# Optimization experiments

Hardware: AMD Instinct MI355X
Metric: run time of the kernel (lower is better)

Reference implementation:

```python
import jax, jax.numpy as jnp
import numpy as np

H = 8          # num_heads
EPS = 1e-6     # layernorm epsilon
NEG_INF = -1e9


def _ln(x, g, b):
    m = jnp.mean(x, axis=-1, keepdims=True)
    v = jnp.mean(jnp.square(x - m), axis=-1, keepdims=True)
    return g * (x - m) * jax.lax.rsqrt(v + EPS) + b


def _mha(xq, kv, wq, wk, wv, wo, bias):
    # xq: [B,Tq,D], kv: [B,Tk,D]; weights [D,D]. Returns (out [B,Tq,D], weights [B,H,Tq,Tk]).
    B, Tq, D = xq.shape
    dh = D // H
    q = (xq @ wq) * (dh ** -0.5)
    k = kv @ wk
    v = kv @ wv
    q = q.reshape(B, Tq, H, dh).transpose(0, 2, 1, 3)
    k = k.reshape(B, -1, H, dh).transpose(0, 2, 1, 3)
    v = v.reshape(B, -1, H, dh).transpose(0, 2, 1, 3)
    logits = jnp.einsum('bhqd,bhkd->bhqk', q, k)
    if bias is not None:
        logits = logits + bias
    w = jax.nn.softmax(logits, axis=-1)
    out = jnp.einsum('bhqk,bhkd->bhqd', w, v).transpose(0, 2, 1, 3).reshape(B, Tq, D)
    return out @ wo, w


def setup_inputs() -> dict:
    key = jax.random.key(0)
    ks = jax.random.split(key, 16)
    B, Td, Te, D, F, L = 2, 2048, 2048, 512, 2048, 2
    s = 0.02
    inp = {
        'x': jax.random.normal(ks[0], (B, Td, D), jnp.float32),
        'enc_a': jax.random.normal(ks[1], (B, Te, D), jnp.float32),
        'enc_c': jax.random.normal(ks[2], (B, Te, D), jnp.float32),
        'sa_wq': jax.random.normal(ks[3], (L, D, D), jnp.float32) * s,
        'sa_wk': jax.random.normal(ks[4], (L, D, D), jnp.float32) * s,
        'sa_wv': jax.random.normal(ks[5], (L, D, D), jnp.float32) * s,
        'sa_wo': jax.random.normal(ks[6], (L, D, D), jnp.float32) * s,
        'ed_wq': jax.random.normal(ks[7], (L, D, D), jnp.float32) * s,
        'ed_wk': jax.random.normal(ks[8], (L, D, D), jnp.float32) * s,
        'ed_wv': jax.random.normal(ks[9], (L, D, D), jnp.float32) * s,
        'ed_wo': jax.random.normal(ks[10], (L, D, D), jnp.float32) * s,
        'ffn_w1': jax.random.normal(ks[11], (L, D, F), jnp.float32) * s,
        'ffn_w2': jax.random.normal(ks[12], (L, F, D), jnp.float32) * s,
        'ln1_g': jnp.ones((L, D), jnp.float32), 'ln1_b': jnp.zeros((L, D), jnp.float32),
        'ln2_g': jnp.ones((L, D), jnp.float32), 'ln2_b': jnp.zeros((L, D), jnp.float32),
        'ln3_g': jnp.ones((L, D), jnp.float32), 'ln3_b': jnp.zeros((L, D), jnp.float32),
        'out_g': jnp.ones((D,), jnp.float32), 'out_b': jnp.zeros((D,), jnp.float32),
    }
    return inp


def reference(x, enc_a, enc_c, sa_wq, sa_wk, sa_wv, sa_wo, ed_wq, ed_wk, ed_wv, ed_wo,
              ffn_w1, ffn_w2, ln1_g, ln1_b, ln2_g, ln2_b, ln3_g, ln3_b, out_g, out_b):
    B, T, D = x.shape
    L = sa_wq.shape[0]
    # decoder self-attention causal bias, broadcast over [B,H]
    causal = jnp.where(jnp.tril(jnp.ones((T, T), bool)), 0.0, NEG_INF)[None, None]
    avg = None
    for i in range(L):
        h = _ln(x, ln1_g[i], ln1_b[i])
        y, _ = _mha(h, h, sa_wq[i], sa_wk[i], sa_wv[i], sa_wo[i], causal)
        x = x + y  # residual (dropout inactive at eval)
        h = _ln(x, ln2_g[i], ln2_b[i])
        y0, _ = _mha(h, enc_a, ed_wq[i], ed_wk[i], ed_wv[i], ed_wo[i], None)
        y1, w = _mha(h, enc_c, ed_wq[i], ed_wk[i], ed_wv[i], ed_wo[i], None)
        # original overwrites attn_scores with second call's head-averaged weights
        scores = jnp.mean(w, axis=1) / L
        avg = scores if avg is None else avg + scores
        x = x + y0 + y1
        h = _ln(x, ln3_g[i], ln3_b[i])
        x = x + jax.nn.relu(h @ ffn_w1[i]) @ ffn_w2[i]
    x = _ln(x, out_g, out_b)
    return x, avg
```

## Files before the change

### kernel.cpp

```cpp
#include <hip/hip_runtime.h>
#include <hip/hip_bf16.h>

#define BB 2
#define TT 2048
#define DD 512
#define FF 2048
#define HH 8
#define DH 64
#define LL 2
#define MM (BB*TT)

typedef __attribute__((ext_vector_type(8))) short bf16x8;
typedef __attribute__((ext_vector_type(4))) float f32x4;

__device__ __forceinline__ float bf2f(unsigned short u) {
    return __uint_as_float(((unsigned int)u) << 16);
}
__device__ __forceinline__ unsigned short f2bf(float f) {
    unsigned int u = __float_as_uint(f);
    u += 0x7fffu + ((u >> 16) & 1u);
    return (unsigned short)(u >> 16);
}
__device__ __forceinline__ unsigned int cvtpk(float a, float b) {
    unsigned int r;
    asm("v_cvt_pk_bf16_f32 %0, %1, %2" : "=v"(r) : "v"(a), "v"(b));
    return r;
}
__device__ __forceinline__ void gload16(const void* g, void* l) {
    __builtin_amdgcn_global_load_lds((__attribute__((address_space(1))) void*)g,
                                     (__attribute__((address_space(3))) void*)l, 16, 0, 0);
}

template<bool BF16OUT>
__global__ __launch_bounds__(256) void ln_kernel(const float* __restrict__ x,
                                                 const float* __restrict__ g,
                                                 const float* __restrict__ b,
                                                 void* __restrict__ out)
{
    const int row = blockIdx.x;
    const int tid = threadIdx.x;
    const float2 v = ((const float2*)(x + (size_t)row * DD))[tid];
    float s = v.x + v.y;
    float q = v.x * v.x + v.y * v.y;
    #pragma unroll
    for (int off = 32; off; off >>= 1) {
        s += __shfl_down(s, off);
        q += __shfl_down(q, off);
    }
    __shared__ float ss[4], qq[4];
    const int wid = tid >> 6;
    if ((tid & 63) == 0) { ss[wid] = s; qq[wid] = q; }
    __syncthreads();
    s = ss[0] + ss[1] + ss[2] + ss[3];
    q = qq[0] + qq[1] + qq[2] + qq[3];
    const float mean = s * (1.0f / DD);
    const float var = q * (1.0f / DD) - mean * mean;
    const float inv = rsqrtf(var + 1e-6f);
    const float2 gg = ((const float2*)g)[tid];
    const float2 bb = ((const float2*)b)[tid];
    const float ox = gg.x * (v.x - mean) * inv + bb.x;
    const float oy = gg.y * (v.y - mean) * inv + bb.y;
    if (BF16OUT) {
        const unsigned int pk = cvtpk(ox, oy);
        ((unsigned int*)((unsigned short*)out + (size_t)row * DD))[tid] = pk;
    } else {
        float2 o; o.x = ox; o.y = oy;
        ((float2*)((float*)out + (size_t)row * DD))[tid] = o;
    }
}

struct CvtEJob { const float* s; unsigned short* d; };
struct CvtEJobs2 { CvtEJob j[2]; };

__global__ __launch_bounds__(256) void cvt_kernel(CvtEJobs2 P, int n)
{
    const CvtEJob jb = P.j[blockIdx.z];
    const int i = (blockIdx.x * 256 + threadIdx.x) * 8;
    if (i >= n) return;
    const float4 a = *(const float4*)(jb.s + i);
    const float4 b = *(const float4*)(jb.s + i + 4);
    unsigned int o[4];
    o[0] = cvtpk(a.x, a.y); o[1] = cvtpk(a.z, a.w);
    o[2] = cvtpk(b.x, b.y); o[3] = cvtpk(b.z, b.w);
    *(bf16x8*)(jb.d + i) = *(bf16x8*)o;
}

struct CvtTJob { const float* s; unsigned short* d; int K; int N; };
struct CvtTJobs20 { CvtTJob j[20]; };

__global__ __launch_bounds__(256) void cvtT_kernel(CvtTJobs20 P)
{
    __shared__ float t[32][33];
    const CvtTJob jb = P.j[blockIdx.z];
    const int gk = blockIdx.y << 5, gn = blockIdx.x << 5;
    if (gk >= jb.K || gn >= jb.N) return;
    const int tx = threadIdx.x & 31, ty = threadIdx.x >> 5;
    #pragma unroll
    for (int i = 0; i < 4; ++i)
        t[ty + i * 8][tx] = jb.s[(size_t)(gk + ty + i * 8) * jb.N + gn + tx];
    __syncthreads();
    #pragma unroll
    for (int i = 0; i < 4; ++i)
        jb.d[(size_t)(gn + ty + i * 8) * jb.K + gk + tx] = f2bf(t[tx][ty + i * 8]);
}

struct GemmJob {
    const unsigned short* A;
    const unsigned short* Wt;
    const float* res;
    float* Cf;
    unsigned short* Cb;
    unsigned short* Ct;
    float scale;
    int relu;
};
struct GemmJobs6 { GemmJob j[6]; };

__global__ __launch_bounds__(256, 2) void gemm_mfma(GemmJobs6 P, int M, int N, int K)
{
    __shared__ __align__(16) unsigned char lds[32768];
    const GemmJob jb = P.j[blockIdx.z];
    const int tid = threadIdx.x, lane = tid & 63, w = tid >> 6;
    const int bn = blockIdx.x << 7, bm = blockIdx.y << 7;
    const int wr = (w >> 1) << 6, wc = (w & 1) << 6;
    const size_t strA = (size_t)K * 2;

    f32x4 acc[4][4] = {};
    const int akey = (lane & 7) << 4;
    const int frow = lane & 15;
    const int kq = (lane >> 4) << 4;

    for (int kt = 0; kt < K; kt += 64) {
        __syncthreads();
        #pragma unroll
        for (int c = 0; c < 4; ++c) {
            const int q = c * 4 + w;
            const int o = (q << 10) + (lane << 4);
            const int row = o >> 7;
            const int colb = (o & 127) ^ ((row & 7) << 4);
            gload16((const char*)jb.A + (size_t)(bm + row) * strA + kt * 2 + colb,
                    lds + (q << 10));
            gload16((const char*)jb.Wt + (size_t)(bn + row) * strA + kt * 2 + colb,
                    lds + 16384 + (q << 10));
        }
        asm volatile("s_waitcnt vmcnt(0)" ::: "memory");
        __syncthreads();
        #pragma unroll
        for (int kk = 0; kk < 2; ++kk) {
            bf16x8 av[4], bv[4];
            #pragma unroll
            for (int i = 0; i < 4; ++i) {
                const int rA = wr + (i << 4) + frow;
                av[i] = *(const bf16x8*)(lds + (rA << 7) + ((((kk << 6) + kq)) ^ akey));
                const int rB = wc + (i << 4) + frow;
                bv[i] = *(const bf16x8*)(lds + 16384 + (rB << 7) + ((((kk << 6) + kq)) ^ akey));
            }
            #pragma unroll
            for (int i = 0; i < 4; ++i)
                #pragma unroll
                for (int j = 0; j < 4; ++j)
                    acc[i][j] = __builtin_amdgcn_mfma_f32_16x16x32_bf16(av[i], bv[j], acc[i][j], 0, 0, 0);
        }
    }

    const int crow0 = (lane >> 4) << 2;
    const int ccol = lane & 15;
    if (jb.Ct) {
        #pragma unroll
        for (int i = 0; i < 4; ++i)
            #pragma unroll
            for (int j = 0; j < 4; ++j) {
                const int gm = bm + wr + (i << 4) + crow0;
                const int gn = bn + wc + (j << 4) + ccol;
                const int bI = gm >> 11, t = gm & 2047;
                const int hI = gn >> 6, d = gn & 63;
                uint2 pk;
                pk.x = cvtpk(acc[i][j][0], acc[i][j][1]);
                pk.y = cvtpk(acc[i][j][2], acc[i][j][3]);
                *(uint2*)(jb.Ct + ((size_t)((bI * HH + hI) * DH + d)) * TT + t) = pk;
            }
        return;
    }
    #pragma unroll
    for (int i = 0; i < 4; ++i) {
        #pragma unroll
        for (int j = 0; j < 4; ++j) {
            #pragma unroll
            for (int r = 0; r < 4; ++r) {
                const int gm = bm + wr + (i << 4) + crow0 + r;
                const int gn = bn + wc + (j << 4) + ccol;
                float v = acc[i][j][r] * jb.scale;
                if (jb.relu) v = fmaxf(v, 0.f);
                const size_t idx = (size_t)gm * N + gn;
                if (jb.res) v += jb.res[idx];
                if (jb.Cf) jb.Cf[idx] = v;
                if (jb.Cb) jb.Cb[idx] = f2bf(v);
            }
        }
    }
}

template<bool CAUSAL, bool DUAL, bool STOREML, int NQ>
__global__ __launch_bounds__(256, 2) void flash_mfma(
    const unsigned short* __restrict__ q,
    const unsigned short* __restrict__ ka, const unsigned short* __restrict__ vta,
    const unsigned short* __restrict__ kc, const unsigned short* __restrict__ vtc,
    unsigned short* __restrict__ outa, unsigned short* __restrict__ outc,
    float* __restrict__ ml)
{
    __shared__ __align__(16) char lds[49152];
    const int tid = threadIdx.x;
    const int lane = tid & 63, w = tid >> 6;
    const int g4 = lane >> 4, c = lane & 15;

    constexpr int GX = 32 / NQ;
    const int f = blockIdx.x + GX * (blockIdx.y + 8 * blockIdx.z);
    const int xcd = f & 7;
    const int tt = f >> 3;
    const int jq = tt % GX;
    const int grp = (tt / GX) * 8 + xcd;
    int b, h, which;
    if (DUAL) { which = grp & 1; b = (grp >> 1) & 1; h = grp >> 2; }
    else      { which = 0;       b = grp & 1;        h = grp >> 1; }
    const int q0 = jq * (64 * NQ);
    const int q0w = q0 + w * (16 * NQ);
    const int kendw = q0w + 16 * NQ;

    const unsigned short* k  = (DUAL && which) ? kc : ka;
    const unsigned short* vt = (DUAL && which) ? vtc : vta;
    unsigned short* out = (DUAL && which) ? outc : outa;

    bf16x8 Qf[NQ][2];
    #pragma unroll
    for (int jb = 0; jb < NQ; ++jb) {
        const unsigned short* qp = q + (size_t)(b * TT + q0w + (jb << 4) + c) * DD + h * DH + (g4 << 3);
        Qf[jb][0] = *(const bf16x8*)qp;
        Qf[jb][1] = *(const bf16x8*)(qp + 32);
    }
    const char* kbase = (const char*)(k + (size_t)b * TT * DD + h * DH);
    const char* vtb   = (const char*)(vt + (size_t)(b * HH + h) * DH * TT);
    char* Pw = lds + 32768 + w * (NQ * 2048);
    const int pkey = (c & 7) << 4;

    f32x4 O[NQ][4] = {};
    float mval[NQ], lpart[NQ];
    #pragma unroll
    for (int jb = 0; jb < NQ; ++jb) { mval[jb] = -1e30f; lpart[jb] = 0.f; }

    const int nt = CAUSAL ? ((q0 + 64 * NQ) >> 6) : (TT >> 6);

    auto STAGE = [&](int t, int sel) {
        const int kt = t << 6;
        char* Kb = lds + sel * 8192;
        char* Vb = lds + 16384 + sel * 8192;
        #pragma unroll
        for (int c8 = 0; c8 < 2; ++c8) {
            const int qc = (c8 << 2) + w;
            const int o = (qc << 10) + (lane << 4);
            const int row = o >> 7;
            const int colb = (o & 127) ^ ((row & 7) << 4);
            gload16(kbase + (size_t)(kt + row) * (DD * 2) + colb, Kb + (qc << 10));
            gload16(vtb + (size_t)row * (TT * 2) + kt * 2 + colb, Vb + (qc << 10));
        }
    };

    STAGE(0, 0);
    asm volatile("s_waitcnt vmcnt(0)" ::: "memory");
    __syncthreads();

    for (int t = 0; t < nt; ++t) {
        const int cur = t & 1;
        if (t + 1 < nt) STAGE(t + 1, cur ^ 1);
        const int kt = t << 6;

        if (!CAUSAL || kt < kendw) {
            const char* Kb = lds + cur * 8192;
            const char* Vb = lds + 16384 + cur * 8192;

            f32x4 s[NQ][4] = {};
            #pragma unroll
            for (int kk = 0; kk < 2; ++kk) {
                bf16x8 av[4];
                #pragma unroll
                for (int i = 0; i < 4; ++i) {
                    const int r = (i << 4) + c;
                    av[i] = *(const bf16x8*)(Kb + (r << 7) + (((kk << 6) + (g4 << 4)) ^ ((r & 7) << 4)));
                }
                #pragma unroll
                for (int i = 0; i < 4; ++i)
                    #pragma unroll
                    for (int jb = 0; jb < NQ; ++jb)
                        s[jb][i] = __builtin_amdgcn_mfma_f32_16x16x32_bf16(av[i], Qf[jb][kk], s[jb][i], 0, 0, 0);
            }

            #pragma unroll
            for (int jb = 0; jb < NQ; ++jb) {
                const int qbase = q0w + (jb << 4);
                if (CAUSAL && kt + 63 > qbase) {
                    #pragma unroll
                    for (int i = 0; i < 4; ++i)
                        #pragma unroll
                        for (int r = 0; r < 4; ++r)
                            if (kt + (i << 4) + (g4 << 2) + r > qbase + c) s[jb][i][r] = -1e30f;
                }
                float pmax = -1e30f;
                #pragma unroll
                for (int i = 0; i < 4; ++i)
                    #pragma unroll
                    for (int r = 0; r < 4; ++r) pmax = fmaxf(pmax, s[jb][i][r]);
                if (__any(pmax > mval[jb] + 11.f)) {
                    float mx = fmaxf(pmax, __shfl_xor(pmax, 16));
                    mx = fmaxf(mx, __shfl_xor(mx, 32));
                    const float mn = fmaxf(mval[jb], mx);
                    const float scf = exp2f(mval[jb] - mn);
                    lpart[jb] *= scf;
                    #pragma unroll
                    for (int r = 0; r < 4; ++r) {
                        const float fr = __shfl(scf, (g4 << 2) + r);
                        #pragma unroll
                        for (int jj = 0; jj < 4; ++jj) O[jb][jj][r] *= fr;
                    }
                    mval[jb] = mn;
                }
                float ps = 0.f;
                #pragma unroll
                for (int i = 0; i < 4; ++i)
                    #pragma unroll
                    for (int r = 0; r < 4; ++r) {
                        const float p = exp2f(s[jb][i][r] - mval[jb]);
                        s[jb][i][r] = p;
                        ps += p;
                    }
                lpart[jb] += ps;
                #pragma unroll
                for (int i = 0; i < 4; ++i) {
                    uint2 pk;
                    pk.x = cvtpk(s[jb][i][0], s[jb][i][1]);
                    pk.y = cvtpk(s[jb][i][2], s[jb][i][3]);
                    const int baddr = (((jb << 4) + c) << 7) + (((i << 4) + (g4 << 2)) << 1);
                    *(uint2*)(Pw + (baddr ^ pkey)) = pk;
                }
            }
            asm volatile("s_waitcnt lgkmcnt(0)" ::: "memory");
            __builtin_amdgcn_sched_barrier(0);

            #pragma unroll
            for (int kk = 0; kk < 2; ++kk) {
                bf16x8 pa[NQ];
                #pragma unroll
                for (int jb = 0; jb < NQ; ++jb)
                    pa[jb] = *(const bf16x8*)(Pw + (((((jb << 4) + c) << 7) + (kk << 6) + (g4 << 4)) ^ pkey));
                #pragma unroll
                for (int jj = 0; jj < 4; ++jj) {
                    const int d = (jj << 4) + c;
                    const bf16x8 vb = *(const bf16x8*)(Vb + (d << 7) + (((kk << 6) + (g4 << 4)) ^ ((d & 7) << 4)));
                    #pragma unroll
                    for (int jb = 0; jb < NQ; ++jb)
                        O[jb][jj] = __builtin_amdgcn_mfma_f32_16x16x32_bf16(pa[jb], vb, O[jb][jj], 0, 0, 0);
                }
            }
        }

        asm volatile("s_waitcnt vmcnt(0)" ::: "memory");
        __syncthreads();
    }

    #pragma unroll
    for (int jb = 0; jb < NQ; ++jb) {
        float l2 = lpart[jb] + __shfl_xor(lpart[jb], 16);
        const float ltot = l2 + __shfl_xor(l2, 32);
        float invL[4];
        #pragma unroll
        for (int r = 0; r < 4; ++r) invL[r] = 1.f / __shfl(ltot, (g4 << 2) + r);
        #pragma unroll
        for (int jj = 0; jj < 4; ++jj)
            #pragma unroll
            for (int r = 0; r < 4; ++r) {
                const int qr = q0w + (jb << 4) + (g4 << 2) + r;
                out[(size_t)(b * TT + qr) * DD + h * DH + (jj << 4) + c] = f2bf(O[jb][jj][r] * invL[r]);
            }
        if (STOREML && (!DUAL || which == 1) && lane < 16) {
            const size_t mi = (((size_t)b * HH + h) * TT + q0w + (jb << 4) + lane) * 2;
            ml[mi] = mval[jb];
            ml[mi + 1] = ltot;
        }
    }
}

__global__ __launch_bounds__(256) void sum_bf16_kernel(const unsigned short* __restrict__ a,
                                                       const unsigned short* __restrict__ b,
                                                       unsigned short* __restrict__ o, int n)
{
    const int i = (blockIdx.x * 256 + threadIdx.x) * 8;
    if (i >= n) return;
    const bf16x8 av = *(const bf16x8*)(a + i);
    const bf16x8 bv = *(const bf16x8*)(b + i);
    unsigned int ov[4];
    #pragma unroll
    for (int e = 0; e < 4; ++e) {
        const float lo = bf2f(((const unsigned short*)&av)[2 * e]) + bf2f(((const unsigned short*)&bv)[2 * e]);
        const float hi = bf2f(((const unsigned short*)&av)[2 * e + 1]) + bf2f(((const unsigned short*)&bv)[2 * e + 1]);
        ov[e] = cvtpk(lo, hi);
    }
    *(bf16x8*)(o + i) = *(bf16x8*)ov;
}

__global__ __launch_bounds__(64) void avg_mfma_kernel(const unsigned short* __restrict__ qm,
                                                      const unsigned short* __restrict__ kcm,
                                                      const float* __restrict__ ml,
                                                      float* __restrict__ avg, int first)
{
    __shared__ __align__(16) unsigned char ldsQ[8192];
    __shared__ __align__(16) unsigned char ldsK[8192];
    __shared__ float sM[8][64];
    __shared__ float sIL[8][64];
    const int lane = threadIdx.x;
    const int kt0 = blockIdx.x << 6, q0 = blockIdx.y << 6, b = blockIdx.z;

    #pragma unroll
    for (int h = 0; h < 8; ++h) {
        const float* mp = ml + (((size_t)(b * HH + h) * TT) + q0 + lane) * 2;
        sM[h][lane] = mp[0];
        sIL[h][lane] = 1.f / mp[1];
    }

    float avac[4][4][4] = {};
    const int akey = (lane & 7) << 4;
    const int frow = lane & 15;
    const int kq = (lane >> 4) << 4;
    const int crow0 = (lane >> 4) << 2;

    for (int h = 0; h < 8; ++h) {
        __syncthreads();
        #pragma unroll
        for (int c = 0; c < 8; ++c) {
            const int o = (c << 10) + (lane << 4);
            const int row = o >> 7;
            const int colb = (o & 127) ^ ((row & 7) << 4);
            gload16((const char*)qm + ((size_t)(b * TT + q0 + row) * DD + h * DH) * 2 + colb,
                    ldsQ + (c << 10));
            gload16((const char*)kcm + ((size_t)(b * TT + kt0 + row) * DD + h * DH) * 2 + colb,
                    ldsK + (c << 10));
        }
        asm volatile("s_waitcnt vmcnt(0)" ::: "memory");
        __syncthreads();
        f32x4 s[4][4] = {};
        #pragma unroll
        for (int kk = 0; kk < 2; ++kk) {
            bf16x8 qv[4], kv[4];
            #pragma unroll
            for (int i = 0; i < 4; ++i) {
                qv[i] = *(const bf16x8*)(ldsQ + (((i << 4) + frow) << 7) + (((kk << 6) + kq) ^ akey));
                kv[i] = *(const bf16x8*)(ldsK + (((i << 4) + frow) << 7) + (((kk << 6) + kq) ^ akey));
            }
            #pragma unroll
            for (int i = 0; i < 4; ++i)
                #pragma unroll
                for (int j = 0; j < 4; ++j)
                    s[i][j] = __builtin_amdgcn_mfma_f32_16x16x32_bf16(qv[i], kv[j], s[i][j], 0, 0, 0);
        }
        #pragma unroll
        for (int i = 0; i < 4; ++i)
            #pragma unroll
            for (int j = 0; j < 4; ++j)
                #pragma unroll
                for (int r = 0; r < 4; ++r) {
                    const int qr = (i << 4) + crow0 + r;
                    avac[i][j][r] += exp2f(s[i][j][r] - sM[h][qr]) * sIL[h][qr];
                }
    }

    float* dst = avg + ((size_t)b * TT + q0) * TT + kt0;
    #pragma unroll
    for (int i = 0; i < 4; ++i)
        #pragma unroll
        for (int j = 0; j < 4; ++j)
            #pragma unroll
            for (int r = 0; r < 4; ++r) {
                const int qr = (i << 4) + crow0 + r;
                const int kc = (j << 4) + (lane & 15);
                const float v = avac[i][j][r] * (1.f / (HH * LL));
                float* p = dst + (size_t)qr * TT + kc;
                *p = first ? v : (*p + v);
            }
}

extern "C" void kernel_launch(void* const* d_in, const int* in_sizes, int n_in,
                              void* d_out, int out_size, void* d_ws, size_t ws_size,
                              hipStream_t stream)
{
    const float* x_in   = (const float*)d_in[0];
    const float* enc_a  = (const float*)d_in[1];
    const float* enc_c  = (const float*)d_in[2];
    const float* sa_wq0 = (const float*)d_in[3];
    const float* sa_wk0 = (const float*)d_in[4];
    const float* sa_wv0 = (const float*)d_in[5];
    const float* sa_wo0 = (const float*)d_in[6];
    const float* ed_wq0 = (const float*)d_in[7];
    const float* ed_wk0 = (const float*)d_in[8];
    const float* ed_wv0 = (const float*)d_in[9];
    const float* ed_wo0 = (const float*)d_in[10];
    const float* ffn_w10 = (const float*)d_in[11];
    const float* ffn_w20 = (const float*)d_in[12];
    const float* ln1_g0 = (const float*)d_in[13];
    const float* ln1_b0 = (const float*)d_in[14];
    const float* ln2_g0 = (const float*)d_in[15];
    const float* ln2_b0 = (const float*)d_in[16];
    const float* ln3_g0 = (const float*)d_in[17];
    const float* ln3_b0 = (const float*)d_in[18];
    const float* out_g  = (const float*)d_in[19];
    const float* out_b  = (const float*)d_in[20];

    const size_t NTD = (size_t)MM * DD;
    const size_t MB = 1u << 20;
    char* W = (char*)d_ws;
    float*          x_buf   = (float*)(W);
    unsigned short* h_bf    = (unsigned short*)(W + 8 * MB);
    unsigned short* q_bf    = (unsigned short*)(W + 12 * MB);
    unsigned short* k1_bf   = (unsigned short*)(W + 16 * MB);
    unsigned short* vt1     = (unsigned short*)(W + 20 * MB);
    unsigned short* k2_bf   = (unsigned short*)(W + 24 * MB);
    unsigned short* vt2     = (unsigned short*)(W + 28 * MB);
    unsigned short* attnA   = (unsigned short*)(W + 32 * MB);
    unsigned short* attnC   = (unsigned short*)(W + 36 * MB);
    float*          ml_buf  = (float*)(W + 40 * MB);
    unsigned short* encA_bf = (unsigned short*)(W + 41 * MB);
    unsigned short* encC_bf = (unsigned short*)(W + 45 * MB);
    unsigned short* wbf     = (unsigned short*)(W + 49 * MB);
    unsigned short* ffn_bf  = q_bf;
    unsigned short* attnS   = h_bf;

    unsigned short* w1t = wbf + (size_t)16 * DD * DD;
    unsigned short* w2t = w1t + (size_t)2 * DD * FF;
    auto wd = [&](int l, int which) { return wbf + ((size_t)(l * 8 + which)) * DD * DD; };

    float* x_out   = (float*)d_out;
    float* avg_out = (float*)d_out + NTD;

    hipMemcpyAsync(x_buf, x_in, NTD * sizeof(float), hipMemcpyDeviceToDevice, stream);

    {
        CvtTJobs20 J{};
        const float* srcs[8] = {sa_wq0, sa_wk0, sa_wv0, sa_wo0, ed_wq0, ed_wk0, ed_wv0, ed_wo0};
        for (int l = 0; l < LL; ++l)
            for (int t = 0; t < 8; ++t)
                J.j[l * 8 + t] = {srcs[t] + (size_t)l * DD * DD, wd(l, t), DD, DD};
        for (int l = 0; l < LL; ++l) {
            J.j[16 + l] = {ffn_w10 + (size_t)l * DD * FF, w1t + (size_t)l * FF * DD, DD, FF};
            J.j[18 + l] = {ffn_w20 + (size_t)l * FF * DD, w2t + (size_t)l * DD * FF, FF, DD};
        }
        cvtT_kernel<<<dim3(FF / 32, FF / 32, 20), 256, 0, stream>>>(J);
    }
    {
        CvtEJobs2 J{};
        J.j[0] = {enc_a, encA_bf};
        J.j[1] = {enc_c, encC_bf};
        cvt_kernel<<<dim3(NTD / 8 / 256, 1, 2), 256, 0, stream>>>(J, (int)NTD);
    }

    const dim3 flashSelfG(32, HH, BB);
    const dim3 flashCrossG(16, HH, BB * 2);
    const dim3 avgG(TT / 64, TT / 64, BB);
    const float qscale = 0.125f * 1.4426950408889634f;

    for (int i = 0; i < LL; ++i) {
        const size_t fOff = (size_t)i * DD * FF;
        const size_t lOff = (size_t)i * DD;

        ln_kernel<true><<<MM, 256, 0, stream>>>(x_buf, ln1_g0 + lOff, ln1_b0 + lOff, h_bf);
        {
            GemmJobs6 J{};
            J.j[0] = {h_bf, wd(i, 0), nullptr, nullptr, q_bf, nullptr, qscale, 0};
            J.j[1] = {h_bf, wd(i, 1), nullptr, nullptr, k1_bf, nullptr, 1.f, 0};
            J.j[2] = {h_bf, wd(i, 2), nullptr, nullptr, nullptr, vt1, 1.f, 0};
            gemm_mfma<<<dim3(DD / 128, MM / 128, 3), 256, 0, stream>>>(J, MM, DD, DD);
        }
        flash_mfma<true, false, false, 1><<<flashSelfG, 256, 0, stream>>>(
            q_bf, k1_bf, vt1, nullptr, nullptr, attnA, nullptr, nullptr);
        {
            GemmJobs6 J{};
            J.j[0] = {attnA, wd(i, 3), x_buf, x_buf, nullptr, nullptr, 1.f, 0};
            gemm_mfma<<<dim3(DD / 128, MM / 128, 1), 256, 0, stream>>>(J, MM, DD, DD);
        }

        ln_kernel<true><<<MM, 256, 0, stream>>>(x_buf, ln2_g0 + lOff, ln2_b0 + lOff, h_bf);
        {
            GemmJobs6 J{};
            J.j[0] = {h_bf,    wd(i, 4), nullptr, nullptr, q_bf, nullptr, qscale, 0};
            J.j[1] = {encA_bf, wd(i, 5), nullptr, nullptr, k1_bf, nullptr, 1.f, 0};
            J.j[2] = {encA_bf, wd(i, 6), nullptr, nullptr, nullptr, vt1, 1.f, 0};
            J.j[3] = {encC_bf, wd(i, 5), nullptr, nullptr, k2_bf, nullptr, 1.f, 0};
            J.j[4] = {encC_bf, wd(i, 6), nullptr, nullptr, nullptr, vt2, 1.f, 0};
            gemm_mfma<<<dim3(DD / 128, MM / 128, 5), 256, 0, stream>>>(J, MM, DD, DD);
        }
        flash_mfma<false, true, true, 2><<<flashCrossG, 256, 0, stream>>>(
            q_bf, k1_bf, vt1, k2_bf, vt2, attnA, attnC, ml_buf);
        sum_bf16_kernel<<<NTD / 8 / 256, 256, 0, stream>>>(attnA, attnC, attnS, (int)NTD);
        avg_mfma_kernel<<<avgG, 64, 0, stream>>>(q_bf, k2_bf, ml_buf, avg_out, (i == 0) ? 1 : 0);
        {
            GemmJobs6 J{};
            J.j[0] = {attnS, wd(i, 7), x_buf, x_buf, nullptr, nullptr, 1.f, 0};
            gemm_mfma<<<dim3(DD / 128, MM / 128, 1), 256, 0, stream>>>(J, MM, DD, DD);
        }

        ln_kernel<true><<<MM, 256, 0, stream>>>(x_buf, ln3_g0 + lOff, ln3_b0 + lOff, h_bf);
        {
            GemmJobs6 J{};
            J.j[0] = {h_bf, w1t + fOff, nullptr, nullptr, ffn_bf, nullptr, 1.f, 1};
            gemm_mfma<<<dim3(FF / 128, MM / 128, 1), 256, 0, stream>>>(J, MM, FF, DD);
        }
        {
            GemmJobs6 J{};
            J.j[0] = {ffn_bf, w2t + fOff, x_buf, x_buf, nullptr, nullptr, 1.f, 0};
            gemm_mfma<<<dim3(DD / 128, MM / 128, 1), 256, 0, stream>>>(J, MM, DD, FF);
        }
    }

    ln_kernel<false><<<MM, 256, 0, stream>>>(x_buf, out_g, out_b, x_out);
}
```

Before: 658.7 us.

## Split flash attention over two KV halves and merge partials in a combine kernel

Each flash attention block now handles only half of the key/value tiles, doubling the grid, and writes unnormalized bf16 partial outputs plus per-row max/sum into scratch buffers. A new merge kernel rescales and combines the two halves, also summing the two cross-attention streams and emitting the row statistics needed by the averaging kernel. This replaces the separate bf16 sum kernel and raises the occupancy hints. The aim is more parallelism and better load balance, especially for the causal self-attention, at the cost of extra global traffic for partials and an added launch. Storing unnormalized partials in bf16 may also lose some precision.

```diff
diff --git a/kernel.cpp b/kernel.cpp
--- a/kernel.cpp
+++ b/kernel.cpp
@@ -200,24 +200,25 @@
     }
 }
 
-template<bool CAUSAL, bool DUAL, bool STOREML, int NQ>
-__global__ __launch_bounds__(256, 2) void flash_mfma(
+template<bool CAUSAL, bool DUAL, int NQ>
+__global__ __launch_bounds__(256, (NQ == 1) ? 4 : 3) void flash_mfma(
     const unsigned short* __restrict__ q,
     const unsigned short* __restrict__ ka, const unsigned short* __restrict__ vta,
     const unsigned short* __restrict__ kc, const unsigned short* __restrict__ vtc,
-    unsigned short* __restrict__ outa, unsigned short* __restrict__ outc,
-    float* __restrict__ ml)
-{
-    __shared__ __align__(16) char lds[49152];
+    unsigned short* __restrict__ Opart,
+    float* __restrict__ mlpart)
+{
+    __shared__ __align__(16) char lds[(NQ == 1) ? 40960 : 49152];
     const int tid = threadIdx.x;
     const int lane = tid & 63, w = tid >> 6;
     const int g4 = lane >> 4, c = lane & 15;
 
-    constexpr int GX = 32 / NQ;
+    constexpr int GX = (32 / NQ) * 2;
     const int f = blockIdx.x + GX * (blockIdx.y + 8 * blockIdx.z);
     const int xcd = f & 7;
     const int tt = f >> 3;
-    const int jq = tt % GX;
+    const int u = tt % GX;
+    const int half = u & 1, jq = u >> 1;
     const int grp = (tt / GX) * 8 + xcd;
     int b, h, which;
     if (DUAL) { which = grp & 1; b = (grp >> 1) & 1; h = grp >> 2; }
@@ -228,7 +229,9 @@
 
     const unsigned short* k  = (DUAL && which) ? kc : ka;
     const unsigned short* vt = (DUAL && which) ? vtc : vta;
-    unsigned short* out = (DUAL && which) ? outc : outa;
+    const int slot = (DUAL ? (which << 1) : 0) + half;
+    unsigned short* Od = Opart + (size_t)slot * MM * DD;
+    float* mld = mlpart + (size_t)slot * (BB * HH * TT * 2);
 
     bf16x8 Qf[NQ][2];
     #pragma unroll
@@ -247,7 +250,9 @@
     #pragma unroll
     for (int jb = 0; jb < NQ; ++jb) { mval[jb] = -1e30f; lpart[jb] = 0.f; }
 
-    const int nt = CAUSAL ? ((q0 + 64 * NQ) >> 6) : (TT >> 6);
+    const int ntt = CAUSAL ? ((q0 + 64 * NQ) >> 6) : (TT >> 6);
+    const int tBeg = half ? ((ntt + 1) >> 1) : 0;
+    const int tEnd = half ? ntt : ((ntt + 1) >> 1);
 
     auto STAGE = [&](int t, int sel) {
         const int kt = t << 6;
@@ -264,145 +269,159 @@
         }
     };
 
-    STAGE(0, 0);
-    asm volatile("s_waitcnt vmcnt(0)" ::: "memory");
-    __syncthreads();
-
-    for (int t = 0; t < nt; ++t) {
-        const int cur = t & 1;
-        if (t + 1 < nt) STAGE(t + 1, cur ^ 1);
-        const int kt = t << 6;
-
-        if (!CAUSAL || kt < kendw) {
-            const char* Kb = lds + cur * 8192;
-            const char* Vb = lds + 16384 + cur * 8192;
-
-            f32x4 s[NQ][4] = {};
-            #pragma unroll
-            for (int kk = 0; kk < 2; ++kk) {
-                bf16x8 av[4];
+    if (tBeg < tEnd) {
+        STAGE(tBeg, 0);
+        asm volatile("s_waitcnt vmcnt(0)" ::: "memory");
+        __syncthreads();
+
+        for (int t = tBeg; t < tEnd; ++t) {
+            const int cur = (t - tBeg) & 1;
+            if (t + 1 < tEnd) STAGE(t + 1, cur ^ 1);
+            const int kt = t << 6;
+
+            if (!CAUSAL || kt < kendw) {
+                const char* Kb = lds + cur * 8192;
+                const char* Vb = lds + 16384 + cur * 8192;
+
+                f32x4 s[NQ][4] = {};
                 #pragma unroll
-                for (int i = 0; i < 4; ++i) {
-                    const int r = (i << 4) + c;
-                    av[i] = *(const bf16x8*)(Kb + (r << 7) + (((kk << 6) + (g4 << 4)) ^ ((r & 7) << 4)));
-                }
-                #pragma unroll
-                for (int i = 0; i < 4; ++i)
+                for (int kk = 0; kk < 2; ++kk) {
+                    bf16x8 av[4];
                     #pragma unroll
-                    for (int jb = 0; jb < NQ; ++jb)
-                        s[jb][i] = __builtin_amdgcn_mfma_f32_16x16x32_bf16(av[i], Qf[jb][kk], s[jb][i], 0, 0, 0);
-            }
-
-            #pragma unroll
-            for (int jb = 0; jb < NQ; ++jb) {
-                const int qbase = q0w + (jb << 4);
-                if (CAUSAL && kt + 63 > qbase) {
+                    for (int i = 0; i < 4; ++i) {
+                        const int r = (i << 4) + c;
+                        av[i] = *(const bf16x8*)(Kb + (r << 7) + (((kk << 6) + (g4 << 4)) ^ ((r & 7) << 4)));
+                    }
                     #pragma unroll
                     for (int i = 0; i < 4; ++i)
                         #pragma unroll
-                        for (int r = 0; r < 4; ++r)
-                            if (kt + (i << 4) + (g4 << 2) + r > qbase + c) s[jb][i][r] = -1e30f;
+                        for (int jb = 0; jb < NQ; ++jb)
+                            s[jb][i] = __builtin_amdgcn_mfma_f32_16x16x32_bf16(av[i], Qf[jb][kk], s[jb][i], 0, 0, 0);
                 }
-                float pmax = -1e30f;
+
                 #pragma unroll
-                for (int i = 0; i < 4; ++i)
+                for (int jb = 0; jb < NQ; ++jb) {
+                    const int qbase = q0w + (jb << 4);
+                    if (CAUSAL && kt + 63 > qbase) {
+                        #pragma unroll
+                        for (int i = 0; i < 4; ++i)
+                            #pragma unroll
+                            for (int r = 0; r < 4; ++r)
+                                if (kt + (i << 4) + (g4 << 2) + r > qbase + c) s[jb][i][r] = -1e30f;
+                    }
+                    float pmax = -1e30f;
                     #pragma unroll
-                    for (int r = 0; r < 4; ++r) pmax = fmaxf(pmax, s[jb][i][r]);
-                if (__any(pmax > mval[jb] + 11.f)) {
-                    float mx = fmaxf(pmax, __shfl_xor(pmax, 16));
-                    mx = fmaxf(mx, __shfl_xor(mx, 32));
-                    const float mn = fmaxf(mval[jb], mx);
-                    const float scf = exp2f(mval[jb] - mn);
-                    lpart[jb] *= scf;
+                    for (int i = 0; i < 4; ++i)
+                        #pragma unroll
+                        for (int r = 0; r < 4; ++r) pmax = fmaxf(pmax, s[jb][i][r]);
+                    if (__any(pmax > mval[jb] + 11.f)) {
+                        float mx = fmaxf(pmax, __shfl_xor(pmax, 16));
+                        mx = fmaxf(mx, __shfl_xor(mx, 32));
+                        const float mn = fmaxf(mval[jb], mx);
+                        const float scf = exp2f(mval[jb] - mn);
+                        lpart[jb] *= scf;
+                        #pragma unroll
+                        for (int r = 0; r < 4; ++r) {
+                            const float fr = __shfl(scf, (g4 << 2) + r);
+                            #pragma unroll
+                            for (int jj = 0; jj < 4; ++jj) O[jb][jj][r] *= fr;
+                        }
+                        mval[jb] = mn;
+                    }
+                    float ps = 0.f;
                     #pragma unroll
-                    for (int r = 0; r < 4; ++r) {
-                        const float fr = __shfl(scf, (g4 << 2) + r);
+                    for (int i = 0; i < 4; ++i)
                         #pragma unroll
-                        for (int jj = 0; jj < 4; ++jj) O[jb][jj][r] *= fr;
+                        for (int r = 0; r < 4; ++r) {
+                            const float p = exp2f(s[jb][i][r] - mval[jb]);
+                            s[jb][i][r] = p;
+                            ps += p;
+                        }
+                    lpart[jb] += ps;
+                    #pragma unroll
+                    for (int i = 0; i < 4; ++i) {
+                        uint2 pk;
+                        pk.x = cvtpk(s[jb][i][0], s[jb][i][1]);
+                        pk.y = cvtpk(s[jb][i][2], s[jb][i][3]);
+                        const int baddr = (((jb << 4) + c) << 7) + (((i << 4) + (g4 << 2)) << 1);
+                        *(uint2*)(Pw + (baddr ^ pkey)) = pk;
                     }
-                    mval[jb] = mn;
                 }
-                float ps = 0.f;
+                asm volatile("s_waitcnt lgkmcnt(0)" ::: "memory");
+                __builtin_amdgcn_sched_barrier(0);
+
                 #pragma unroll
-                for (int i = 0; i < 4; ++i)
+                for (int kk = 0; kk < 2; ++kk) {
+                    bf16x8 pa[NQ];
                     #pragma unroll
-                    for (int r = 0; r < 4; ++r) {
-                        const float p = exp2f(s[jb][i][r] - mval[jb]);
-                        s[jb][i][r] = p;
-                        ps += p;
+                    for (int jb = 0; jb < NQ; ++jb)
+                        pa[jb] = *(const bf16x8*)(Pw + (((((jb << 4) + c) << 7) + (kk << 6) + (g4 << 4)) ^ pkey));
+                    #pragma unroll
+                    for (int jj = 0; jj < 4; ++jj) {
+                        const int d = (jj << 4) + c;
+                        const bf16x8 vb = *(const bf16x8*)(Vb + (d << 7) + (((kk << 6) + (g4 << 4)) ^ ((d & 7) << 4)));
+                        #pragma unroll
+                        for (int jb = 0; jb < NQ; ++jb)
+                            O[jb][jj] = __builtin_amdgcn_mfma_f32_16x16x32_bf16(pa[jb], vb, O[jb][jj], 0, 0, 0);
                     }
-                lpart[jb] += ps;
-                #pragma unroll
-                for (int i = 0; i < 4; ++i) {
-                    uint2 pk;
-                    pk.x = cvtpk(s[jb][i][0], s[jb][i][1]);
-                    pk.y = cvtpk(s[jb][i][2], s[jb][i][3]);
-                    const int baddr = (((jb << 4) + c) << 7) + (((i << 4) + (g4 << 2)) << 1);
-                    *(uint2*)(Pw + (baddr ^ pkey)) = pk;
                 }
             }
-            asm volatile("s_waitcnt lgkmcnt(0)" ::: "memory");
-            __builtin_amdgcn_sched_barrier(0);
-
-            #pragma unroll
-            for (int kk = 0; kk < 2; ++kk) {
-                bf16x8 pa[NQ];
-                #pragma unroll
-                for (int jb = 0; jb < NQ; ++jb)
-                    pa[jb] = *(const bf16x8*)(Pw + (((((jb << 4) + c) << 7) + (kk << 6) + (g4 << 4)) ^ pkey));
-                #pragma unroll
-                for (int jj = 0; jj < 4; ++jj) {
-                    const int d = (jj << 4) + c;
-                    const bf16x8 vb = *(const bf16x8*)(Vb + (d << 7) + (((kk << 6) + (g4 << 4)) ^ ((d & 7) << 4)));
-                    #pragma unroll
-                    for (int jb = 0; jb < NQ; ++jb)
-                        O[jb][jj] = __builtin_amdgcn_mfma_f32_16x16x32_bf16(pa[jb], vb, O[jb][jj], 0, 0, 0);
-                }
-            }
-        }
-
-        asm volatile("s_waitcnt vmcnt(0)" ::: "memory");
-        __syncthreads();
+
+            asm volatile("s_waitcnt vmcnt(0)" ::: "memory");
+            __syncthreads();
+        }
     }
 
     #pragma unroll
     for (int jb = 0; jb < NQ; ++jb) {
         float l2 = lpart[jb] + __shfl_xor(lpart[jb], 16);
         const float ltot = l2 + __shfl_xor(l2, 32);
-        float invL[4];
-        #pragma unroll
-        for (int r = 0; r < 4; ++r) invL[r] = 1.f / __shfl(ltot, (g4 << 2) + r);
         #pragma unroll
         for (int jj = 0; jj < 4; ++jj)
             #pragma unroll
             for (int r = 0; r < 4; ++r) {
                 const int qr = q0w + (jb << 4) + (g4 << 2) + r;
-                out[(size_t)(b * TT + qr) * DD + h * DH + (jj << 4) + c] = f2bf(O[jb][jj][r] * invL[r]);
+                Od[(size_t)(b * TT + qr) * DD + h * DH + (jj << 4) + c] = f2bf(O[jb][jj][r]);
             }
-        if (STOREML && (!DUAL || which == 1) && lane < 16) {
+        if (lane < 16) {
             const size_t mi = (((size_t)b * HH + h) * TT + q0w + (jb << 4) + lane) * 2;
-            ml[mi] = mval[jb];
-            ml[mi + 1] = ltot;
-        }
-    }
-}
-
-__global__ __launch_bounds__(256) void sum_bf16_kernel(const unsigned short* __restrict__ a,
-                                                       const unsigned short* __restrict__ b,
-                                                       unsigned short* __restrict__ o, int n)
-{
-    const int i = (blockIdx.x * 256 + threadIdx.x) * 8;
-    if (i >= n) return;
-    const bf16x8 av = *(const bf16x8*)(a + i);
-    const bf16x8 bv = *(const bf16x8*)(b + i);
-    unsigned int ov[4];
-    #pragma unroll
-    for (int e = 0; e < 4; ++e) {
-        const float lo = bf2f(((const unsigned short*)&av)[2 * e]) + bf2f(((const unsigned short*)&bv)[2 * e]);
-        const float hi = bf2f(((const unsigned short*)&av)[2 * e + 1]) + bf2f(((const unsigned short*)&bv)[2 * e + 1]);
-        ov[e] = cvtpk(lo, hi);
-    }
-    *(bf16x8*)(o + i) = *(bf16x8*)ov;
+            mld[mi] = mval[jb];
+            mld[mi + 1] = ltot;
+        }
+    }
+}
+
+template<int NS, bool STOREML>
+__global__ __launch_bounds__(256) void merge_kernel(
+    const unsigned short* __restrict__ Opart, const float* __restrict__ mlpart,
+    unsigned short* __restrict__ out, float* __restrict__ ml_out)
+{
+    const int row = blockIdx.x;
+    const int b = row >> 11, rt = row & 2047;
+    const int t = threadIdx.x;
+    const int d0 = t << 1, h = d0 >> 6;
+    float acc0 = 0.f, acc1 = 0.f;
+    float Ms = 0.f, Ls = 0.f;
+    #pragma unroll
+    for (int s = 0; s < NS; ++s) {
+        const size_t mb = ((size_t)(b * HH + h) * TT + rt) * 2;
+        const float* mp0 = mlpart + (size_t)(s * 2 + 0) * (BB * HH * TT * 2) + mb;
+        const float* mp1 = mlpart + (size_t)(s * 2 + 1) * (BB * HH * TT * 2) + mb;
+        const float m0 = mp0[0], l0 = mp0[1], m1 = mp1[0], l1 = mp1[1];
+        const float M = fmaxf(m0, m1);
+        const float a0 = exp2f(m0 - M), a1 = exp2f(m1 - M);
+        const float inv = 1.f / (a0 * l0 + a1 * l1);
+        const unsigned short* p0 = Opart + (size_t)(s * 2 + 0) * MM * DD + (size_t)row * DD + d0;
+        const unsigned short* p1 = Opart + (size_t)(s * 2 + 1) * MM * DD + (size_t)row * DD + d0;
+        acc0 += (a0 * bf2f(p0[0]) + a1 * bf2f(p1[0])) * inv;
+        acc1 += (a0 * bf2f(p0[1]) + a1 * bf2f(p1[1])) * inv;
+        if (STOREML && s == NS - 1) { Ms = M; Ls = a0 * l0 + a1 * l1; }
+    }
+    ((unsigned int*)(out + (size_t)row * DD))[t] = cvtpk(acc0, acc1);
+    if (STOREML && (d0 & 63) == 0) {
+        float* mo = ml_out + ((size_t)(b * HH + h) * TT + rt) * 2;
+        mo[0] = Ms; mo[1] = Ls;
+    }
 }
 
 __global__ __launch_bounds__(64) void avg_mfma_kernel(const unsigned short* __restrict__ qm,
@@ -522,13 +541,14 @@
     unsigned short* k2_bf   = (unsigned short*)(W + 24 * MB);
     unsigned short* vt2     = (unsigned short*)(W + 28 * MB);
     unsigned short* attnA   = (unsigned short*)(W + 32 * MB);
-    unsigned short* attnC   = (unsigned short*)(W + 36 * MB);
+    unsigned short* attnS   = (unsigned short*)(W + 36 * MB);
     float*          ml_buf  = (float*)(W + 40 * MB);
     unsigned short* encA_bf = (unsigned short*)(W + 41 * MB);
     unsigned short* encC_bf = (unsigned short*)(W + 45 * MB);
     unsigned short* wbf     = (unsigned short*)(W + 49 * MB);
+    unsigned short* Opart   = (unsigned short*)(W + 68 * MB);
+    float*          mlpart  = (float*)(W + 84 * MB);
     unsigned short* ffn_bf  = q_bf;
-    unsigned short* attnS   = h_bf;
 
     unsigned short* w1t = wbf + (size_t)16 * DD * DD;
     unsigned short* w2t = w1t + (size_t)2 * DD * FF;
@@ -558,8 +578,8 @@
         cvt_kernel<<<dim3(NTD / 8 / 256, 1, 2), 256, 0, stream>>>(J, (int)NTD);
     }
 
-    const dim3 flashSelfG(32, HH, BB);
-    const dim3 flashCrossG(16, HH, BB * 2);
+    const dim3 flashSelfG(64, HH, BB);
+    const dim3 flashCrossG(32, HH, BB * 2);
     const dim3 avgG(TT / 64, TT / 64, BB);
     const float qscale = 0.125f * 1.4426950408889634f;
 
@@ -575,8 +595,9 @@
             J.j[2] = {h_bf, wd(i, 2), nullptr, nullptr, nullptr, vt1, 1.f, 0};
             gemm_mfma<<<dim3(DD / 128, MM / 128, 3), 256, 0, stream>>>(J, MM, DD, DD);
         }
-        flash_mfma<true, false, false, 1><<<flashSelfG, 256, 0, stream>>>(
-            q_bf, k1_bf, vt1, nullptr, nullptr, attnA, nullptr, nullptr);
+        flash_mfma<true, false, 1><<<flashSelfG, 256, 0, stream>>>(
+            q_bf, k1_bf, vt1, nullptr, nullptr, Opart, mlpart);
+        merge_kernel<1, false><<<MM, 256, 0, stream>>>(Opart, mlpart, attnA, nullptr);
         {
             GemmJobs6 J{};
             J.j[0] = {attnA, wd(i, 3), x_buf, x_buf, nullptr, nullptr, 1.f, 0};
@@ -593,9 +614,9 @@
             J.j[4] = {encC_bf, wd(i, 6), nullptr, nullptr, nullptr, vt2, 1.f, 0};
             gemm_mfma<<<dim3(DD / 128, MM / 128, 5), 256, 0, stream>>>(J, MM, DD, DD);
         }
-        flash_mfma<false, true, true, 2><<<flashCrossG, 256, 0, stream>>>(
-            q_bf, k1_bf, vt1, k2_bf, vt2, attnA, attnC, ml_buf);
-        sum_bf16_kernel<<<NTD / 8 / 256, 256, 0, stream>>>(attnA, attnC, attnS, (int)NTD);
+        flash_mfma<false, true, 2><<<flashCrossG, 256, 0, stream>>>(
+            q_bf, k1_bf, vt1, k2_bf, vt2, Opart, mlpart);
+        merge_kernel<2, true><<<MM, 256, 0, stream>>>(Opart, mlpart, attnS, ml_buf);
         avg_mfma_kernel<<<avgG, 64, 0, stream>>>(q_bf, k2_bf, ml_buf, avg_out, (i == 0) ? 1 : 0);
         {
             GemmJobs6 J{};
```

Result: faster. 644.8 us (-2.1%).
